# Performance work log

Hardware: AMD Instinct MI355X
Metric: run time of the kernel (lower is better)

The kernel has to match this reference:

```python
import jax, jax.numpy as jnp
import numpy as np

EPS = 1e-6


def setup_inputs() -> dict:
    key = jax.random.key(0)
    kq, kk, kv = jax.random.split(key, 3)
    B, H, S, D = 1, 16, 2048, 64
    q = jax.random.normal(kq, (B, H, S, D), dtype=jnp.float32)
    k = jax.random.normal(kk, (B, H, S, D), dtype=jnp.float32)
    v = jax.random.normal(kv, (B, H, S, D), dtype=jnp.float32)
    return {"q": q, "k": k, "v": v}


def reference(q, k, v):
    # Rebased linear attention: squared scaled QK score, causal mask,
    # normalized by running row-sum (not softmax).
    B, H, S, D = q.shape
    scale = D ** (-0.5)
    # [B,H,S,S] raw scores
    s = jnp.einsum("bhid,bhjd->bhij", q, k) * scale
    s2 = s * s
    causal = jnp.tril(jnp.ones((S, S), dtype=bool))  # k_idx <= q_idx
    s2 = jnp.where(causal, s2, jnp.zeros((), dtype=s2.dtype))
    z = jnp.sum(s2, axis=-1)  # [B,H,S]
    o = jnp.einsum("bhij,bhjd->bhid", s2, v)
    return o / (z[..., None] + EPS)
```

## Files before the change

### kernel.cpp

```cpp
#include <hip/hip_runtime.h>

typedef __attribute__((ext_vector_type(8))) short bf16x8;
typedef __attribute__((ext_vector_type(16))) float f32x16;

#define SLEN 2048
#define DDIM 64
#define NH 16
#define KEPS 1e-6f
#define TILE_B 16384

__device__ __forceinline__ unsigned cvtpk(float lo, float hi) {
    unsigned r;
    asm("v_cvt_pk_bf16_f32 %0, %1, %2" : "=v"(r) : "v"(lo), "v"(hi));
    return r;
}
__device__ __forceinline__ f32x16 mfma32x32(bf16x8 a, bf16x8 b, f32x16 c) {
    return __builtin_amdgcn_mfma_f32_32x32x16_bf16(a, b, c, 0, 0, 0);
}
__device__ __forceinline__ void gload16(const void* g, void* l) {
    __builtin_amdgcn_global_load_lds(
        (const __attribute__((address_space(1))) unsigned*)g,
        (__attribute__((address_space(3))) unsigned*)l, 16, 0, 0);
}

__global__ void __launch_bounds__(256) prep_kernel(
    const float* __restrict__ K, const float* __restrict__ V, char* __restrict__ WS)
{
    const int b  = blockIdx.x;
    const int h  = b >> 5;
    const int kt = b & 31;
    const int t  = threadIdx.x;
    char* chunk = WS + (size_t)b * TILE_B;

    {
        const int j = t >> 2, ks = t & 3, c16 = ks * 16;
        const float* src = K + ((size_t)h * SLEN + kt * 64 + j) * DDIM + c16;
        float4 a = ((const float4*)src)[0], bb = ((const float4*)src)[1];
        float4 c = ((const float4*)src)[2], d = ((const float4*)src)[3];
        uint4 lo = make_uint4(cvtpk(a.x,a.y), cvtpk(a.z,a.w), cvtpk(bb.x,bb.y), cvtpk(bb.z,bb.w));
        uint4 hi = make_uint4(cvtpk(c.x,c.y), cvtpk(c.z,c.w), cvtpk(d.x,d.y), cvtpk(d.z,d.w));
        *(uint4*)(chunk + ((size_t)((ks*2+0)*64 + j)) * 16) = lo;
        *(uint4*)(chunk + ((size_t)((ks*2+1)*64 + j)) * 16) = hi;
    }
    {
        const int j0 = (t & 15) * 4, d0 = (t >> 4) * 4;
        const float* vs = V + ((size_t)h * SLEN + kt * 64 + j0) * DDIM + d0;
        float4 r0 = *(const float4*)(vs);
        float4 r1 = *(const float4*)(vs + DDIM);
        float4 r2 = *(const float4*)(vs + 2 * DDIM);
        float4 r3 = *(const float4*)(vs + 3 * DDIM);
        char* vbase = chunk + 8192;
        const int cv  = j0 >> 3;
        const int tof = j0 & 7;
#pragma unroll
        for (int c = 0; c < 4; ++c) {
            uint2 pk = make_uint2(
                cvtpk(((const float*)&r0)[c], ((const float*)&r1)[c]),
                cvtpk(((const float*)&r2)[c], ((const float*)&r3)[c]));
            *(uint2*)(vbase + (size_t)(cv * 64 + d0 + c) * 16 + tof * 2) = pk;
        }
    }
}

__global__ void __launch_bounds__(256) attn_main(
    const float* __restrict__ Q, const char* __restrict__ WS, float* __restrict__ O)
{
    __shared__ __align__(16) char smem[2][TILE_B];

    const int bid = blockIdx.x;
    const int h   = bid & 15;
    const int u   = bid >> 4;
    const int g   = (u < 16) ? u : (47 - u);

    const int tid  = threadIdx.x;
    const int w    = tid >> 6;
    const int lane = tid & 63;
    const int il   = lane & 31;
    const int hi   = lane >> 5;
    const int qhalf = w >> 1;
    const int jb    = w & 1;

    const int q0 = g * 64 + qhalf * 32;

    const float* __restrict__ Qh = Q + (size_t)h * SLEN * DDIM;
    float* __restrict__ Oh = O + (size_t)h * SLEN * DDIM;
    const char* __restrict__ WSh = WS + (size_t)h * 32 * TILE_B;

    bf16x8 qf[4];
#pragma unroll
    for (int ks = 0; ks < 4; ++ks) {
        const float* src = Qh + (size_t)(q0 + il) * DDIM + ks * 16 + hi * 8;
        float4 a = *reinterpret_cast<const float4*>(src);
        float4 b = *reinterpret_cast<const float4*>(src + 4);
        uint4 uq = make_uint4(cvtpk(a.x, a.y), cvtpk(a.z, a.w),
                              cvtpk(b.x, b.y), cvtpk(b.z, b.w));
        qf[ks] = *reinterpret_cast<bf16x8*>(&uq);
    }

    f32x16 o0, o1;
#pragma unroll
    for (int rr = 0; rr < 16; ++rr) { o0[rr] = 0.f; o1[rr] = 0.f; }
    float z = 0.f;

    auto stage = [&](int buf, int kt) {
        const char* gs = WSh + (size_t)kt * TILE_B + w * 4096 + lane * 16;
        char* ls = &smem[buf][w * 4096];
#pragma unroll
        for (int i = 0; i < 4; ++i)
            gload16(gs + i * 1024, ls + i * 1024);
    };

    const int kbase = (jb * 32 + il) * 16;
    const int vbase = 8192 + (jb * 4 + hi) * 1024 + il * 16;

    const int ktend = g - ((jb > qhalf) ? 1 : 0);

    stage(0, 0);
    __syncthreads();

    for (int kt = 0; kt <= g; ++kt) {
        const int cur = kt & 1;
        if (kt < g) stage(cur ^ 1, kt + 1);

        if (kt <= ktend) {
            const char* base = smem[cur];
            bf16x8 kf0 = *(const bf16x8*)(base + 0 * 1024 + hi * 1024 + kbase);
            bf16x8 kf1 = *(const bf16x8*)(base + 2 * 1024 + hi * 1024 + kbase);
            bf16x8 kf2 = *(const bf16x8*)(base + 4 * 1024 + hi * 1024 + kbase);
            bf16x8 kf3 = *(const bf16x8*)(base + 6 * 1024 + hi * 1024 + kbase);

            __builtin_amdgcn_s_setprio(1);
            f32x16 sv;
#pragma unroll
            for (int rr = 0; rr < 16; ++rr) sv[rr] = 0.f;
            sv = mfma32x32(kf0, qf[0], sv);
            sv = mfma32x32(kf1, qf[1], sv);
            sv = mfma32x32(kf2, qf[2], sv);
            sv = mfma32x32(kf3, qf[3], sv);
            __builtin_amdgcn_s_setprio(0);

            const bool tri = (kt == g) && (jb == qhalf);
#pragma unroll
            for (int rr = 0; rr < 16; ++rr) {
                float x = sv[rr];
                x = x * x * 0.015625f;
                if (tri) {
                    int jl = (rr & 3) + 8 * (rr >> 2) + 4 * hi;
                    if (jl > il) x = 0.f;
                }
                sv[rr] = x;
            }
            {
                float a0 = (sv[0] + sv[1]) + (sv[2] + sv[3]);
                float a1 = (sv[4] + sv[5]) + (sv[6] + sv[7]);
                float a2 = (sv[8] + sv[9]) + (sv[10] + sv[11]);
                float a3 = (sv[12] + sv[13]) + (sv[14] + sv[15]);
                z += (a0 + a1) + (a2 + a3);
            }

            __builtin_amdgcn_s_setprio(1);
            {
                unsigned X  = cvtpk(sv[0], sv[1]);
                unsigned Xp = cvtpk(sv[2], sv[3]);
                unsigned Y  = cvtpk(sv[4], sv[5]);
                unsigned Yp = cvtpk(sv[6], sv[7]);
                asm("v_permlane32_swap_b32 %0, %1" : "+v"(X), "+v"(Y));
                asm("v_permlane32_swap_b32 %0, %1" : "+v"(Xp), "+v"(Yp));
                uint4 aw = make_uint4(X, Xp, Y, Yp);
                bf16x8 pf = *reinterpret_cast<bf16x8*>(&aw);
                bf16x8 va = *(const bf16x8*)(base + vbase + 0 * 2048 + 0 * 512);
                bf16x8 vb = *(const bf16x8*)(base + vbase + 0 * 2048 + 1 * 512);
                o0 = mfma32x32(pf, va, o0);
                o1 = mfma32x32(pf, vb, o1);
            }
            {
                unsigned X  = cvtpk(sv[8],  sv[9]);
                unsigned Xp = cvtpk(sv[10], sv[11]);
                unsigned Y  = cvtpk(sv[12], sv[13]);
                unsigned Yp = cvtpk(sv[14], sv[15]);
                asm("v_permlane32_swap_b32 %0, %1" : "+v"(X), "+v"(Y));
                asm("v_permlane32_swap_b32 %0, %1" : "+v"(Xp), "+v"(Yp));
                uint4 aw = make_uint4(X, Xp, Y, Yp);
                bf16x8 pf = *reinterpret_cast<bf16x8*>(&aw);
                bf16x8 va = *(const bf16x8*)(base + vbase + 1 * 2048 + 0 * 512);
                bf16x8 vb = *(const bf16x8*)(base + vbase + 1 * 2048 + 1 * 512);
                o0 = mfma32x32(pf, va, o0);
                o1 = mfma32x32(pf, vb, o1);
            }
            __builtin_amdgcn_s_setprio(0);
        }

        __syncthreads();
    }

    z += __shfl_xor(z, 32);
    float* red = (float*)smem;
    if (jb == 1) {
        float* r = red + (size_t)((qhalf * 64 + lane) * 33);
#pragma unroll
        for (int rr = 0; rr < 16; ++rr) { r[rr] = o0[rr]; r[16 + rr] = o1[rr]; }
        r[32] = z;
    }
    __syncthreads();
    if (jb == 0) {
        const float* r = red + (size_t)((qhalf * 64 + lane) * 33);
#pragma unroll
        for (int rr = 0; rr < 16; ++rr) { o0[rr] += r[rr]; o1[rr] += r[16 + rr]; }
        z += r[32];

        const float invl = 1.f / (z + KEPS);
#pragma unroll
        for (int rr = 0; rr < 16; ++rr) {
            const int rl = (rr & 3) + 8 * (rr >> 2) + 4 * hi;
            const float inv = __shfl(invl, rl);
            Oh[(size_t)(q0 + rl) * DDIM + il]      = o0[rr] * inv;
            Oh[(size_t)(q0 + rl) * DDIM + 32 + il] = o1[rr] * inv;
        }
    }
}

__global__ void __launch_bounds__(256) attn_fp32(
    const float* __restrict__ Q, const float* __restrict__ K,
    const float* __restrict__ V, float* __restrict__ O)
{
    __shared__ float red[2][64][33];
    const int bid = blockIdx.x;
    const int h   = bid & 15;
    const int u   = bid >> 4;
    const int g   = (u < 16) ? u : (47 - u);
    const int tid  = threadIdx.x;
    const int w    = tid >> 6;
    const int lane = tid & 63;
    const int il   = lane & 31;
    const int hi   = lane >> 5;
    const int qhalf = w >> 1;
    const int jb    = w & 1;
    const int q0 = g * 64 + qhalf * 32;

    const float* Qh = Q + (size_t)h * SLEN * DDIM;
    const float* Kh = K + (size_t)h * SLEN * DDIM;
    const float* Vh = V + (size_t)h * SLEN * DDIM;
    float* Oh = O + (size_t)h * SLEN * DDIM;

    bf16x8 qf[4];
#pragma unroll
    for (int ks = 0; ks < 4; ++ks) {
        const float* src = Qh + (size_t)(q0 + il) * DDIM + ks * 16 + hi * 8;
        float4 a = *reinterpret_cast<const float4*>(src);
        float4 b = *reinterpret_cast<const float4*>(src + 4);
        uint4 uq = make_uint4(cvtpk(a.x, a.y), cvtpk(a.z, a.w),
                              cvtpk(b.x, b.y), cvtpk(b.z, b.w));
        qf[ks] = *reinterpret_cast<bf16x8*>(&uq);
    }
    f32x16 o0, o1;
#pragma unroll
    for (int rr = 0; rr < 16; ++rr) { o0[rr] = 0.f; o1[rr] = 0.f; }
    float z = 0.f;
    const int ktend = g - ((jb > qhalf) ? 1 : 0);

    for (int kt = 0; kt <= ktend; ++kt) {
        f32x16 sv;
#pragma unroll
        for (int rr = 0; rr < 16; ++rr) sv[rr] = 0.f;
#pragma unroll
        for (int ks = 0; ks < 4; ++ks) {
            const float* src = Kh + (size_t)(kt * 64 + jb * 32 + il) * DDIM + ks * 16 + hi * 8;
            float4 a = *reinterpret_cast<const float4*>(src);
            float4 b = *reinterpret_cast<const float4*>(src + 4);
            uint4 uk = make_uint4(cvtpk(a.x, a.y), cvtpk(a.z, a.w),
                                  cvtpk(b.x, b.y), cvtpk(b.z, b.w));
            sv = mfma32x32(*reinterpret_cast<bf16x8*>(&uk), qf[ks], sv);
        }
        const bool tri = (kt == g) && (jb == qhalf);
#pragma unroll
        for (int rr = 0; rr < 16; ++rr) {
            float x = sv[rr];
            x = x * x * 0.015625f;
            if (tri) {
                int jl = (rr & 3) + 8 * (rr >> 2) + 4 * hi;
                if (jl > il) x = 0.f;
            }
            sv[rr] = x;
            z += x;
        }
#pragma unroll
        for (int s16 = 0; s16 < 2; ++s16) {
            unsigned X  = cvtpk(sv[8*s16+0], sv[8*s16+1]);
            unsigned Xp = cvtpk(sv[8*s16+2], sv[8*s16+3]);
            unsigned Y  = cvtpk(sv[8*s16+4], sv[8*s16+5]);
            unsigned Yp = cvtpk(sv[8*s16+6], sv[8*s16+7]);
            asm("v_permlane32_swap_b32 %0, %1" : "+v"(X), "+v"(Y));
            asm("v_permlane32_swap_b32 %0, %1" : "+v"(Xp), "+v"(Yp));
            uint4 aw = make_uint4(X, Xp, Y, Yp);
            bf16x8 pf = *reinterpret_cast<bf16x8*>(&aw);
#pragma unroll
            for (int dt = 0; dt < 2; ++dt) {
                float v8[8];
#pragma unroll
                for (int t = 0; t < 8; ++t)
                    v8[t] = Vh[(size_t)(kt * 64 + jb * 32 + s16 * 16 + hi * 8 + t) * DDIM + dt * 32 + il];
                uint4 uv = make_uint4(cvtpk(v8[0], v8[1]), cvtpk(v8[2], v8[3]),
                                      cvtpk(v8[4], v8[5]), cvtpk(v8[6], v8[7]));
                bf16x8 vf = *reinterpret_cast<bf16x8*>(&uv);
                if (dt == 0) o0 = mfma32x32(pf, vf, o0);
                else         o1 = mfma32x32(pf, vf, o1);
            }
        }
    }

    z += __shfl_xor(z, 32);
    if (jb == 1) {
        float* r = &red[qhalf][lane][0];
#pragma unroll
        for (int rr = 0; rr < 16; ++rr) { r[rr] = o0[rr]; r[16 + rr] = o1[rr]; }
        r[32] = z;
    }
    __syncthreads();
    if (jb == 0) {
        const float* r = &red[qhalf][lane][0];
#pragma unroll
        for (int rr = 0; rr < 16; ++rr) { o0[rr] += r[rr]; o1[rr] += r[16 + rr]; }
        z += r[32];
        const float invl = 1.f / (z + KEPS);
#pragma unroll
        for (int rr = 0; rr < 16; ++rr) {
            const int rl = (rr & 3) + 8 * (rr >> 2) + 4 * hi;
            const float inv = __shfl(invl, rl);
            Oh[(size_t)(q0 + rl) * DDIM + il]      = o0[rr] * inv;
            Oh[(size_t)(q0 + rl) * DDIM + 32 + il] = o1[rr] * inv;
        }
    }
}

extern "C" void kernel_launch(void* const* d_in, const int* in_sizes, int n_in,
                              void* d_out, int out_size, void* d_ws, size_t ws_size,
                              hipStream_t stream) {
    const float* q = (const float*)d_in[0];
    const float* k = (const float*)d_in[1];
    const float* v = (const float*)d_in[2];
    float* o = (float*)d_out;

    const size_t need = (size_t)NH * 32 * TILE_B;
    if (ws_size >= need) {
        char* ws = (char*)d_ws;
        hipLaunchKernelGGL(prep_kernel, dim3(NH * 32), dim3(256), 0, stream, k, v, ws);
        hipLaunchKernelGGL(attn_main, dim3(512), dim3(256), 0, stream, q, ws, o);
    } else {
        hipLaunchKernelGGL(attn_fp32, dim3(512), dim3(256), 0, stream, q, k, v, o);
    }
}
```

Baseline: 33.04 us.

## Triple-buffer K/V staging with vmcnt waits and transpose V via LDS in prep

The main loop moves from double to triple LDS buffering. It prefetches two tiles ahead, uses explicit s_waitcnt vmcnt and a single barrier per iteration instead of two __syncthreads, which is meant to hide global-to-LDS latency. The prep kernel now transposes V through a padded shared-memory tile so global reads and writes are coalesced, and it interleaves block-to-head mapping. This raises LDS use to 48KB per block, which may reduce occupancy. The vmcnt counting relies on exactly four loads per stage.

```diff
diff --git a/kernel.cpp b/kernel.cpp
--- a/kernel.cpp
+++ b/kernel.cpp
@@ -8,7 +8,13 @@
 #define NH 16
 #define KEPS 1e-6f
 #define TILE_B 16384
-
+#define PSTR 72
+
+__device__ __forceinline__ short f2bf(float x) {
+    unsigned u = __float_as_uint(x);
+    unsigned r = (u + 0x7FFFu + ((u >> 16) & 1u)) >> 16;
+    return (short)r;
+}
 __device__ __forceinline__ unsigned cvtpk(float lo, float hi) {
     unsigned r;
     asm("v_cvt_pk_bf16_f32 %0, %1, %2" : "=v"(r) : "v"(lo), "v"(hi));
@@ -26,14 +32,18 @@
 __global__ void __launch_bounds__(256) prep_kernel(
     const float* __restrict__ K, const float* __restrict__ V, char* __restrict__ WS)
 {
+    __shared__ short vt[64 * PSTR];
     const int b  = blockIdx.x;
-    const int h  = b >> 5;
-    const int kt = b & 31;
+    const int h  = b & 15;
+    const int kt = b >> 4;
     const int t  = threadIdx.x;
-    char* chunk = WS + (size_t)b * TILE_B;
+    const int j  = t >> 2;
+    const int ks = t & 3;
+    const int c16 = ks * 16;
+
+    char* chunk = WS + ((size_t)h * 32 + kt) * TILE_B;
 
     {
-        const int j = t >> 2, ks = t & 3, c16 = ks * 16;
         const float* src = K + ((size_t)h * SLEN + kt * 64 + j) * DDIM + c16;
         float4 a = ((const float4*)src)[0], bb = ((const float4*)src)[1];
         float4 c = ((const float4*)src)[2], d = ((const float4*)src)[3];
@@ -43,29 +53,30 @@
         *(uint4*)(chunk + ((size_t)((ks*2+1)*64 + j)) * 16) = hi;
     }
     {
-        const int j0 = (t & 15) * 4, d0 = (t >> 4) * 4;
-        const float* vs = V + ((size_t)h * SLEN + kt * 64 + j0) * DDIM + d0;
-        float4 r0 = *(const float4*)(vs);
-        float4 r1 = *(const float4*)(vs + DDIM);
-        float4 r2 = *(const float4*)(vs + 2 * DDIM);
-        float4 r3 = *(const float4*)(vs + 3 * DDIM);
+        const float* src = V + ((size_t)h * SLEN + kt * 64 + j) * DDIM + c16;
+        float4 a = ((const float4*)src)[0], bb = ((const float4*)src)[1];
+        float4 c = ((const float4*)src)[2], d = ((const float4*)src)[3];
+        float f[16] = {a.x,a.y,a.z,a.w, bb.x,bb.y,bb.z,bb.w, c.x,c.y,c.z,c.w, d.x,d.y,d.z,d.w};
+#pragma unroll
+        for (int q = 0; q < 16; ++q)
+            vt[(c16 + q) * PSTR + j] = f2bf(f[q]);
+    }
+    __syncthreads();
+    {
+        const int d  = t >> 2;
+        const int jc = (t & 3) * 16;
+        uint4 lo = *(const uint4*)&vt[d * PSTR + jc];
+        uint4 hi = *(const uint4*)&vt[d * PSTR + jc + 8];
         char* vbase = chunk + 8192;
-        const int cv  = j0 >> 3;
-        const int tof = j0 & 7;
-#pragma unroll
-        for (int c = 0; c < 4; ++c) {
-            uint2 pk = make_uint2(
-                cvtpk(((const float*)&r0)[c], ((const float*)&r1)[c]),
-                cvtpk(((const float*)&r2)[c], ((const float*)&r3)[c]));
-            *(uint2*)(vbase + (size_t)(cv * 64 + d0 + c) * 16 + tof * 2) = pk;
-        }
+        *(uint4*)(vbase + (size_t)(((jc >> 4) * 2 + 0) * 64 + d) * 16) = lo;
+        *(uint4*)(vbase + (size_t)(((jc >> 4) * 2 + 1) * 64 + d) * 16) = hi;
     }
 }
 
 __global__ void __launch_bounds__(256) attn_main(
     const float* __restrict__ Q, const char* __restrict__ WS, float* __restrict__ O)
 {
-    __shared__ __align__(16) char smem[2][TILE_B];
+    __shared__ __align__(16) char smem[3][TILE_B];
 
     const int bid = blockIdx.x;
     const int h   = bid & 15;
@@ -116,11 +127,17 @@
     const int ktend = g - ((jb > qhalf) ? 1 : 0);
 
     stage(0, 0);
-    __syncthreads();
+    if (g >= 1) stage(1, 1);
 
     for (int kt = 0; kt <= g; ++kt) {
-        const int cur = kt & 1;
-        if (kt < g) stage(cur ^ 1, kt + 1);
+        const int cur = kt % 3;
+
+        if (kt < g) asm volatile("s_waitcnt vmcnt(4)" ::: "memory");
+        else        asm volatile("s_waitcnt vmcnt(0)" ::: "memory");
+        __builtin_amdgcn_s_barrier();
+        __builtin_amdgcn_sched_barrier(0);
+
+        if (kt + 2 <= g) stage((kt + 2) % 3, kt + 2);
 
         if (kt <= ktend) {
             const char* base = smem[cur];
@@ -189,10 +206,9 @@
             }
             __builtin_amdgcn_s_setprio(0);
         }
-
-        __syncthreads();
-    }
-
+    }
+
+    __syncthreads();
     z += __shfl_xor(z, 32);
     float* red = (float*)smem;
     if (jb == 1) {
```

Measured after the change: 36.22 us. 1.1x slower.
